# Performance work log

Measured on AMD Instinct MI355X. Metric: run time of the kernel, lower is better.

## Reference

```python
import jax, jax.numpy as jnp
import numpy as np

B, CIN, COUT, SDIM, H, W, K = 16, 512, 512, 512, 32, 32, 3
LIN_SCALE = 1.0 / np.sqrt(SDIM)            # EqualLinear equalized-lr scale
CONV_SCALE = 1.0 / np.sqrt(CIN * K * K)    # ModulatedConv2d equalized-lr scale
ACT_GAIN = np.sqrt(2.0)                    # EqualLeakyReLU gain
NEG_SLOPE = 0.2
EPS = 1e-8


def setup_inputs() -> dict:
    key = jax.random.key(0)
    ks = jax.random.split(key, 6)
    x = jax.random.normal(ks[0], (B, CIN, H, W), jnp.float32)
    w = jax.random.normal(ks[1], (B, SDIM), jnp.float32)
    noise = jax.random.normal(ks[2], (B, 1, 2 * H, 2 * W), jnp.float32)
    lin_w = jax.random.normal(ks[3], (CIN, SDIM), jnp.float32)
    lin_b = jnp.ones((CIN,), jnp.float32)  # nn.init.ones_(self.style.bias)
    conv_w = jax.random.normal(ks[4], (COUT, CIN, K, K), jnp.float32)
    noise_weight = jnp.float32(0.1)  # scalar noise strength (nonzero so the noise path is exercised)
    return {"x": x, "w": w, "noise": noise, "lin_w": lin_w, "lin_b": lin_b,
            "conv_w": conv_w, "noise_weight": noise_weight}


def reference(x, w, noise, lin_w, lin_b, conv_w, noise_weight):
    b, c, h, wd = x.shape
    x = jax.image.resize(x, (b, c, 2 * h, 2 * wd), method="bilinear")
    # 2) style = EqualLinear(w): [B, CIN]
    s = w @ (lin_w * LIN_SCALE).T + lin_b
    # 3) modulated conv: modulate input, shared-weight conv, demodulate output
    wk = conv_w * CONV_SCALE                       # [COUT, CIN, K, K]
    xm = x * s[:, :, None, None]                   # per-sample input modulation
    y = jax.lax.conv_general_dilated(
        xm, wk, window_strides=(1, 1), padding=((1, 1), (1, 1)),
        dimension_numbers=("NCHW", "OIHW", "NCHW"))
    # demod[b,o] = 1/sqrt(sum_{i,k,l} (wk[o,i,k,l]*s[b,i])^2 + eps)
    demod = jax.lax.rsqrt(jnp.einsum("oikl,bi->bo", wk * wk, s * s) + EPS)
    y = y * demod[:, :, None, None]
    # 4) noise injection + equalized leaky relu
    y = y + noise_weight * noise
    return jnp.where(y >= 0, y, NEG_SLOPE * y) * ACT_GAIN
```

## Files before the change

### kernel.cpp

```cpp
#include <hip/hip_runtime.h>
#include <hip/hip_bf16.h>

#define B_ 16
#define CIN_ 512
#define COUT_ 512
#define SDIM_ 512
#define HIN_ 32
#define WIN_ 32
#define HOUT_ 64
#define WOUT_ 64

#define LIN_SCALE_C 0.044194173824159216f
#define CONV_SCALE_C 0.014731391274719742f

typedef short short8 __attribute__((ext_vector_type(8)));
typedef float f32x4 __attribute__((ext_vector_type(4)));

typedef const __attribute__((address_space(1))) void* gptr_t;
typedef __attribute__((address_space(3))) void* sptr_t;

__device__ __forceinline__ void glds16(const void* g, void* l) {
    __builtin_amdgcn_global_load_lds((gptr_t)g, (sptr_t)l, 16, 0, 0);
}

__global__ void style_kernel(const float* __restrict__ w, const float* __restrict__ lin_w,
                             const float* __restrict__ lin_b, float* __restrict__ s) {
    const int gw   = (blockIdx.x * 256 + threadIdx.x) >> 6;
    const int lane = threadIdx.x & 63;
    const int b = gw >> 9, i = gw & 511;
    const float* wr = w + b * SDIM_;
    const float* lw = lin_w + i * SDIM_;
    float acc = 0.f;
    #pragma unroll
    for (int j = 0; j < 8; ++j) acc += wr[lane + j * 64] * lw[lane + j * 64];
    #pragma unroll
    for (int off = 32; off; off >>= 1) acc += __shfl_xor(acc, off);
    if (lane == 0) s[b * CIN_ + i] = acc * LIN_SCALE_C + lin_b[i];
}

__global__ void prep_weights(const float* __restrict__ conv_w, __hip_bfloat16* __restrict__ w2,
                             float* __restrict__ wsq, float* __restrict__ zbuf) {
    const int o = blockIdx.x;
    for (int i = threadIdx.x; i < CIN_; i += 256) {
        const float* src = conv_w + (o * CIN_ + i) * 9;
        float ss = 0.f;
        #pragma unroll
        for (int kk = 0; kk < 9; ++kk) {
            float v = src[kk] * CONV_SCALE_C;
            ss += v * v;
            w2[o * 4608 + kk * 512 + i] = __float2bfloat16(v);
        }
        wsq[o * CIN_ + i] = ss;
    }
    if (blockIdx.x == 0 && threadIdx.x < 64) zbuf[threadIdx.x] = 0.f;
}

__global__ void demod_kernel(const float* __restrict__ wsq, const float* __restrict__ s,
                             float* __restrict__ demod) {
    const int gw   = (blockIdx.x * 256 + threadIdx.x) >> 6;
    const int lane = threadIdx.x & 63;
    const int b = gw >> 9, o = gw & 511;
    const float* sr = s + b * CIN_;
    const float* wr = wsq + o * CIN_;
    float acc = 0.f;
    #pragma unroll
    for (int j = 0; j < 8; ++j) {
        float sv = sr[lane + j * 64];
        acc += wr[lane + j * 64] * sv * sv;
    }
    #pragma unroll
    for (int off = 32; off; off >>= 1) acc += __shfl_xor(acc, off);
    if (lane == 0) demod[b * COUT_ + o] = 1.0f / sqrtf(acc + 1e-8f);
}

__global__ void upsample_mod_kernel(const float* __restrict__ x, const float* __restrict__ s,
                                    __hip_bfloat16* __restrict__ xq) {
    __shared__ float xs[10 * 32 * 33];
    const int ht = blockIdx.x;
    const int ct = blockIdx.y;
    const int b  = blockIdx.z;
    const int tid = threadIdx.x;
    const int ho0 = ht * 16, h0 = ht * 8, c0 = ct * 32;

    for (int idx = tid; idx < 10240; idx += 256) {
        int ch = idx / 320; int rem = idx - ch * 320;
        int rr = rem >> 5;  int col = rem & 31;
        int srow = h0 - 1 + rr; srow = min(max(srow, 0), 31);
        xs[(rr * 32 + col) * 33 + ch] = x[((b * CIN_ + c0 + ch) * HIN_ + srow) * WIN_ + col];
    }
    __syncthreads();

    for (int e = tid; e < 32768; e += 256) {
        int c = e & 31; int rest = e >> 5; int wo = rest & 63; int hr = rest >> 6;
        int ri0 = (hr + (hr & 1)) >> 1;
        float wlo_h = (hr & 1) ? 0.75f : 0.25f;
        int clo = (wo - 2 + (wo & 1)) >> 1;
        float wlo_w = (wo & 1) ? 0.75f : 0.25f;
        int chi = min(clo + 1, 31); clo = max(clo, 0);
        float v0 = xs[(ri0 * 32 + clo) * 33 + c];
        float v1 = xs[(ri0 * 32 + chi) * 33 + c];
        float v2 = xs[((ri0 + 1) * 32 + clo) * 33 + c];
        float v3 = xs[((ri0 + 1) * 32 + chi) * 33 + c];
        float rlo = wlo_w * v0 + (1.f - wlo_w) * v1;
        float rhi = wlo_w * v2 + (1.f - wlo_w) * v3;
        float val = (wlo_h * rlo + (1.f - wlo_h) * rhi) * s[b * CIN_ + c0 + c];
        xq[(((b * HOUT_ + ho0 + hr) * WOUT_) + wo) * CIN_ + c0 + c] = __float2bfloat16(val);
    }
}

__global__ __launch_bounds__(512)
void conv_kernel(const __hip_bfloat16* __restrict__ xq,
                 const __hip_bfloat16* __restrict__ w2,
                 const float* __restrict__ demod,
                 const float* __restrict__ noise,
                 const float* __restrict__ nw_p,
                 float* __restrict__ out,
                 const __hip_bfloat16* __restrict__ zbuf) {
    extern __shared__ __hip_bfloat16 smem[];
    __hip_bfloat16* As = smem;
    __hip_bfloat16* Bs = smem + 16384;

    const int bid = blockIdx.x;
    const int swz = (bid & 7) * 64 + (bid >> 3);
    const int b  = swz >> 5;
    const int mt = (swz >> 4) & 1;
    const int nt = swz & 15;
    const int o0 = mt * 256;
    const int p0 = nt * 256;

    const int tid  = threadIdx.x;
    const int lane = tid & 63;
    const int wave = tid >> 6;
    const int wm = wave >> 2, wn = wave & 3;

    const int srow = tid >> 2;
    const int schk = (((tid & 3) ^ ((tid >> 3) & 3))) * 8;
    const int aoff = (o0 + srow) * 4608 + schk;
    const int brow_lo = nt * 4 + (srow >> 6);
    const int bcol = srow & 63;
    const int sdst = tid * 8;

    const int lrow = lane & 15;
    const int pko = ((lane >> 4) ^ ((lrow >> 1) & 3)) * 8;
    const int ard = (wm * 128 + lrow) * 32 + pko;
    const int brd = (wn * 64 + lrow) * 32 + pko;

    f32x4 acc[8][4] = {};

    #define STAGE_A(u, h) \
        glds16(w2 + aoff + (h) * 589824 + (u) * 32, As + (((u) & 1) << 13) + ((h) << 12) + sdst)
    #define STAGE_B(u, h, dh, dw, i0) do { \
        int rr_ = brow_lo + (h) * 2 + (dh); \
        int cc_ = bcol + (dw); \
        bool v_ = ((unsigned)rr_ < 64u) && ((unsigned)cc_ < 64u); \
        const __hip_bfloat16* src_ = v_ ? xq + ((b * 64 + rr_) * 64 + cc_) * 512 + (i0) + schk : zbuf; \
        glds16(src_, Bs + (((u) & 1) << 13) + ((h) << 12) + sdst); \
    } while (0)

    STAGE_A(0, 0); STAGE_A(0, 1); STAGE_B(0, 0, -1, -1, 0); STAGE_B(0, 1, -1, -1, 0);
    asm volatile("s_waitcnt vmcnt(0)" ::: "memory");
    __builtin_amdgcn_s_barrier();

    #pragma unroll 4
    for (int t = 0; t < 144; ++t) {
        const int u = t + 1;
        if (u < 144) {
            const int kk = u >> 4;
            const int i0 = (u & 15) << 5;
            const int kd = (kk * 11) >> 5;
            const int dh = kd - 1, dw = kk - kd * 3 - 1;
            STAGE_A(u, 0); STAGE_A(u, 1);
            STAGE_B(u, 0, dh, dw, i0); STAGE_B(u, 1, dh, dw, i0);
        }

        const int slot = (t & 1) << 13;
        short8 a[8], bf[4];
        #pragma unroll
        for (int m = 0; m < 8; ++m)
            a[m] = *(const short8*)(As + slot + ard + m * 512);
        #pragma unroll
        for (int n = 0; n < 4; ++n)
            bf[n] = *(const short8*)(Bs + slot + brd + n * 512);

        __builtin_amdgcn_s_setprio(1);
        #pragma unroll
        for (int m = 0; m < 8; ++m)
            #pragma unroll
            for (int n = 0; n < 4; ++n)
                acc[m][n] = __builtin_amdgcn_mfma_f32_16x16x32_bf16(a[m], bf[n], acc[m][n], 0, 0, 0);
        __builtin_amdgcn_s_setprio(0);

        asm volatile("s_waitcnt vmcnt(0)" ::: "memory");
        __builtin_amdgcn_s_barrier();
    }
    #undef STAGE_A
    #undef STAGE_B

    const float nwv = nw_p[0];
    const int colp = lane & 15;
    const int rgrp = (lane >> 4) * 4;
    float nz[4];
    #pragma unroll
    for (int ni = 0; ni < 4; ++ni)
        nz[ni] = noise[b * 4096 + p0 + wn * 64 + ni * 16 + colp] * nwv;
    #pragma unroll
    for (int mi = 0; mi < 8; ++mi) {
        const int obase = o0 + wm * 128 + mi * 16 + rgrp;
        float dm[4];
        #pragma unroll
        for (int j = 0; j < 4; ++j) dm[j] = demod[b * COUT_ + obase + j];
        #pragma unroll
        for (int ni = 0; ni < 4; ++ni) {
            const int pix = p0 + wn * 64 + ni * 16 + colp;
            #pragma unroll
            for (int j = 0; j < 4; ++j) {
                float v = acc[mi][ni][j] * dm[j] + nz[ni];
                v = (v >= 0.f ? v : 0.2f * v) * 1.4142135623730951f;
                out[(b * COUT_ + obase + j) * 4096 + pix] = v;
            }
        }
    }
}

extern "C" void kernel_launch(void* const* d_in, const int* in_sizes, int n_in,
                              void* d_out, int out_size, void* d_ws, size_t ws_size,
                              hipStream_t stream) {
    const float* x      = (const float*)d_in[0];
    const float* w      = (const float*)d_in[1];
    const float* noise  = (const float*)d_in[2];
    const float* lin_w  = (const float*)d_in[3];
    const float* lin_b  = (const float*)d_in[4];
    const float* conv_w = (const float*)d_in[5];
    const float* nw     = (const float*)d_in[6];
    float* out = (float*)d_out;

    char* ws = (char*)d_ws;
    __hip_bfloat16* xq = (__hip_bfloat16*)ws;
    __hip_bfloat16* w2 = (__hip_bfloat16*)(ws + 67108864);
    float* s     = (float*)(ws + 71827456);
    float* demod = (float*)(ws + 71860224);
    float* wsq   = (float*)(ws + 71892992);
    float* zbuf  = (float*)(ws + 72941568);

    static int lds_set = 0;
    if (!lds_set) {
        (void)hipFuncSetAttribute((const void*)conv_kernel,
                                  hipFuncAttributeMaxDynamicSharedMemorySize, 65536);
        lds_set = 1;
    }

    style_kernel<<<2048, 256, 0, stream>>>(w, lin_w, lin_b, s);
    prep_weights<<<512, 256, 0, stream>>>(conv_w, w2, wsq, zbuf);
    demod_kernel<<<2048, 256, 0, stream>>>(wsq, s, demod);
    upsample_mod_kernel<<<dim3(4, 16, 16), 256, 0, stream>>>(x, s, xq);
    conv_kernel<<<512, 512, 65536, stream>>>(xq, w2, demod, noise, nw, out,
                                             (const __hip_bfloat16*)zbuf);
}
```

Before: 320.0 us.

## Deepen conv LDS ring to four slots with prefetch distance two; vectorize upsample stores

The conv kernel's shared-memory buffers grow from two slots to four (128 KB LDS). Stages are now prefetched two K-steps ahead, and each iteration waits only on the oldest outstanding loads, so global-to-LDS traffic overlaps MFMA work instead of draining to zero every step. The upsample kernel now writes eight bf16 channels per 16-byte store and caches the style scales in shared memory. prep_weights stages conv weights through LDS so the global reads are coalesced. The larger LDS footprint limits occupancy to one block per CU, and correctness depends on the partial vmcnt counting.

```diff
diff --git a/kernel.cpp b/kernel.cpp
--- a/kernel.cpp
+++ b/kernel.cpp
@@ -1,5 +1,6 @@
 #include <hip/hip_runtime.h>
 #include <hip/hip_bf16.h>
+#include <string.h>
 
 #define B_ 16
 #define CIN_ 512
@@ -40,19 +41,22 @@
 
 __global__ void prep_weights(const float* __restrict__ conv_w, __hip_bfloat16* __restrict__ w2,
                              float* __restrict__ wsq, float* __restrict__ zbuf) {
+    __shared__ float xs[4608];
     const int o = blockIdx.x;
-    for (int i = threadIdx.x; i < CIN_; i += 256) {
-        const float* src = conv_w + (o * CIN_ + i) * 9;
+    const int tid = threadIdx.x;
+    for (int idx = tid; idx < 4608; idx += 256) xs[idx] = conv_w[o * 4608 + idx];
+    __syncthreads();
+    for (int i = tid; i < CIN_; i += 256) {
         float ss = 0.f;
         #pragma unroll
         for (int kk = 0; kk < 9; ++kk) {
-            float v = src[kk] * CONV_SCALE_C;
+            float v = xs[i * 9 + kk] * CONV_SCALE_C;
             ss += v * v;
             w2[o * 4608 + kk * 512 + i] = __float2bfloat16(v);
         }
         wsq[o * CIN_ + i] = ss;
     }
-    if (blockIdx.x == 0 && threadIdx.x < 64) zbuf[threadIdx.x] = 0.f;
+    if (blockIdx.x == 0 && tid < 64) zbuf[tid] = 0.f;
 }
 
 __global__ void demod_kernel(const float* __restrict__ wsq, const float* __restrict__ s,
@@ -76,12 +80,14 @@
 __global__ void upsample_mod_kernel(const float* __restrict__ x, const float* __restrict__ s,
                                     __hip_bfloat16* __restrict__ xq) {
     __shared__ float xs[10 * 32 * 33];
+    __shared__ float ssh[32];
     const int ht = blockIdx.x;
     const int ct = blockIdx.y;
     const int b  = blockIdx.z;
     const int tid = threadIdx.x;
     const int ho0 = ht * 16, h0 = ht * 8, c0 = ct * 32;
 
+    if (tid < 32) ssh[tid] = s[b * CIN_ + c0 + tid];
     for (int idx = tid; idx < 10240; idx += 256) {
         int ch = idx / 320; int rem = idx - ch * 320;
         int rr = rem >> 5;  int col = rem & 31;
@@ -90,21 +96,32 @@
     }
     __syncthreads();
 
-    for (int e = tid; e < 32768; e += 256) {
-        int c = e & 31; int rest = e >> 5; int wo = rest & 63; int hr = rest >> 6;
+    for (int e = tid; e < 4096; e += 256) {
+        int c8 = e & 3; int wo = (e >> 2) & 63; int hr = e >> 8;
         int ri0 = (hr + (hr & 1)) >> 1;
         float wlo_h = (hr & 1) ? 0.75f : 0.25f;
         int clo = (wo - 2 + (wo & 1)) >> 1;
         float wlo_w = (wo & 1) ? 0.75f : 0.25f;
         int chi = min(clo + 1, 31); clo = max(clo, 0);
-        float v0 = xs[(ri0 * 32 + clo) * 33 + c];
-        float v1 = xs[(ri0 * 32 + chi) * 33 + c];
-        float v2 = xs[((ri0 + 1) * 32 + clo) * 33 + c];
-        float v3 = xs[((ri0 + 1) * 32 + chi) * 33 + c];
-        float rlo = wlo_w * v0 + (1.f - wlo_w) * v1;
-        float rhi = wlo_w * v2 + (1.f - wlo_w) * v3;
-        float val = (wlo_h * rlo + (1.f - wlo_h) * rhi) * s[b * CIN_ + c0 + c];
-        xq[(((b * HOUT_ + ho0 + hr) * WOUT_) + wo) * CIN_ + c0 + c] = __float2bfloat16(val);
+        const float* r0p = xs + (ri0 * 32) * 33;
+        const float* r1p = xs + ((ri0 + 1) * 32) * 33;
+        short8 v;
+        #pragma unroll
+        for (int q = 0; q < 8; ++q) {
+            const int c = c8 * 8 + q;
+            float v0 = r0p[clo * 33 + c];
+            float v1 = r0p[chi * 33 + c];
+            float v2 = r1p[clo * 33 + c];
+            float v3 = r1p[chi * 33 + c];
+            float rlo = wlo_w * v0 + (1.f - wlo_w) * v1;
+            float rhi = wlo_w * v2 + (1.f - wlo_w) * v3;
+            float val = (wlo_h * rlo + (1.f - wlo_h) * rhi) * ssh[c];
+            __hip_bfloat16 hv = __float2bfloat16(val);
+            unsigned short us;
+            __builtin_memcpy(&us, &hv, 2);
+            v[q] = (short)us;
+        }
+        *(short8*)(xq + (((size_t)(b * 64) + ho0 + hr) * 64 + wo) * 512 + c0 + c8 * 8) = v;
     }
 }
 
@@ -118,7 +135,7 @@
                  const __hip_bfloat16* __restrict__ zbuf) {
     extern __shared__ __hip_bfloat16 smem[];
     __hip_bfloat16* As = smem;
-    __hip_bfloat16* Bs = smem + 16384;
+    __hip_bfloat16* Bs = smem + 32768;
 
     const int bid = blockIdx.x;
     const int swz = (bid & 7) * 64 + (bid >> 3);
@@ -148,22 +165,33 @@
     f32x4 acc[8][4] = {};
 
     #define STAGE_A(u, h) \
-        glds16(w2 + aoff + (h) * 589824 + (u) * 32, As + (((u) & 1) << 13) + ((h) << 12) + sdst)
+        glds16(w2 + aoff + (h) * 589824 + (u) * 32, As + (((u) & 3) << 13) + ((h) << 12) + sdst)
     #define STAGE_B(u, h, dh, dw, i0) do { \
         int rr_ = brow_lo + (h) * 2 + (dh); \
         int cc_ = bcol + (dw); \
         bool v_ = ((unsigned)rr_ < 64u) && ((unsigned)cc_ < 64u); \
         const __hip_bfloat16* src_ = v_ ? xq + ((b * 64 + rr_) * 64 + cc_) * 512 + (i0) + schk : zbuf; \
-        glds16(src_, Bs + (((u) & 1) << 13) + ((h) << 12) + sdst); \
+        glds16(src_, Bs + (((u) & 3) << 13) + ((h) << 12) + sdst); \
     } while (0)
 
-    STAGE_A(0, 0); STAGE_A(0, 1); STAGE_B(0, 0, -1, -1, 0); STAGE_B(0, 1, -1, -1, 0);
-    asm volatile("s_waitcnt vmcnt(0)" ::: "memory");
+    STAGE_A(0, 0); STAGE_A(0, 1); STAGE_B(0, 0, -1, -1, 0);  STAGE_B(0, 1, -1, -1, 0);
+    STAGE_A(1, 0); STAGE_A(1, 1); STAGE_B(1, 0, -1, -1, 32); STAGE_B(1, 1, -1, -1, 32);
+    asm volatile("s_waitcnt vmcnt(4)" ::: "memory");
     __builtin_amdgcn_s_barrier();
 
     #pragma unroll 4
     for (int t = 0; t < 144; ++t) {
-        const int u = t + 1;
+        const int slot = (t & 3) << 13;
+
+        short8 a[8], bf[4];
+        #pragma unroll
+        for (int m = 0; m < 8; ++m)
+            a[m] = *(const short8*)(As + slot + ard + m * 512);
+        #pragma unroll
+        for (int n = 0; n < 4; ++n)
+            bf[n] = *(const short8*)(Bs + slot + brd + n * 512);
+
+        const int u = t + 2;
         if (u < 144) {
             const int kk = u >> 4;
             const int i0 = (u & 15) << 5;
@@ -173,14 +201,9 @@
             STAGE_B(u, 0, dh, dw, i0); STAGE_B(u, 1, dh, dw, i0);
         }
 
-        const int slot = (t & 1) << 13;
-        short8 a[8], bf[4];
-        #pragma unroll
-        for (int m = 0; m < 8; ++m)
-            a[m] = *(const short8*)(As + slot + ard + m * 512);
-        #pragma unroll
-        for (int n = 0; n < 4; ++n)
-            bf[n] = *(const short8*)(Bs + slot + brd + n * 512);
+        if (t < 142) asm volatile("s_waitcnt vmcnt(4)" ::: "memory");
+        else         asm volatile("s_waitcnt vmcnt(0)" ::: "memory");
+        __builtin_amdgcn_s_barrier();
 
         __builtin_amdgcn_s_setprio(1);
         #pragma unroll
@@ -189,9 +212,6 @@
             for (int n = 0; n < 4; ++n)
                 acc[m][n] = __builtin_amdgcn_mfma_f32_16x16x32_bf16(a[m], bf[n], acc[m][n], 0, 0, 0);
         __builtin_amdgcn_s_setprio(0);
-
-        asm volatile("s_waitcnt vmcnt(0)" ::: "memory");
-        __builtin_amdgcn_s_barrier();
     }
     #undef STAGE_A
     #undef STAGE_B
@@ -245,7 +265,7 @@
     static int lds_set = 0;
     if (!lds_set) {
         (void)hipFuncSetAttribute((const void*)conv_kernel,
-                                  hipFuncAttributeMaxDynamicSharedMemorySize, 65536);
+                                  hipFuncAttributeMaxDynamicSharedMemorySize, 131072);
         lds_set = 1;
     }
 
@@ -253,6 +273,6 @@
     prep_weights<<<512, 256, 0, stream>>>(conv_w, w2, wsq, zbuf);
     demod_kernel<<<2048, 256, 0, stream>>>(wsq, s, demod);
     upsample_mod_kernel<<<dim3(4, 16, 16), 256, 0, stream>>>(x, s, xq);
-    conv_kernel<<<512, 512, 65536, stream>>>(xq, w2, demod, noise, nw, out,
-                                             (const __hip_bfloat16*)zbuf);
-}
+    conv_kernel<<<512, 512, 131072, stream>>>(xq, w2, demod, noise, nw, out,
+                                              (const __hip_bfloat16*)zbuf);
+}
```

Result: faster. 292.7 us (-8.5%).
